# Kernel tuning notes

Measured on AMD Instinct MI355X. Metric: run time of the kernel, lower is better.

The kernel has to match this reference:

```python
import jax, jax.numpy as jnp
import numpy as np
from math import sqrt

IMG_SIZE = 512
FMAP = IMG_SIZE // 32            # 16
RATIOS = (1.0 / 3.0, 0.5, 1.0, 2.0, 3.0)
SCALE = 0.35
N_CLASSES = 21                   # class 0 = background
MIN_SCORE = 0.01
MAX_OVERLAP = 0.45
BATCH = 16


def make_anchors():
    # mirrors DetectionBaseline.create_anchors (cx, cy, w, h in [0,1])
    anchors = []
    for i in range(FMAP):
        for j in range(FMAP):
            cx = (j + 0.5) / FMAP
            cy = (i + 0.5) / FMAP
            for r in RATIOS:
                anchors.append([cx, cy, SCALE * sqrt(r), SCALE / sqrt(r)])
    return jnp.clip(jnp.asarray(anchors, dtype=jnp.float32), 0.0, 1.0)


def setup_inputs() -> dict:
    key = jax.random.key(0)
    k1, k2 = jax.random.split(key)
    A = FMAP * FMAP * len(RATIOS)  # 1280 anchors
    return {
        "predicted_locs": jax.random.normal(k1, (BATCH, A, 4), dtype=jnp.float32),
        "predicted_scores": jax.random.normal(k2, (BATCH, A, N_CLASSES), dtype=jnp.float32),
        "anchors": make_anchors(),
        "top_k": 200,
    }


def _pairwise_iou(boxes):
    # boxes: [B, A, 4] xyxy -> iou [B, A, A]
    area = (boxes[..., 2] - boxes[..., 0]) * (boxes[..., 3] - boxes[..., 1])
    lt = jnp.maximum(boxes[:, :, None, :2], boxes[:, None, :, :2])
    rb = jnp.minimum(boxes[:, :, None, 2:], boxes[:, None, :, 2:])
    wh = jnp.clip(rb - lt, 0.0, None)
    inter = wh[..., 0] * wh[..., 1]
    union = area[:, :, None] + area[:, None, :] - inter
    return inter / union


def reference(predicted_locs, predicted_scores, anchors, top_k):
    B, A, C = predicted_scores.shape
    Cf = C - 1  # foreground classes
    scores = jax.nn.softmax(predicted_scores, axis=2)  # [B, A, C]

    # standard SSD decode (gcxgcywh -> cxcywh -> xyxy)
    cxcy = predicted_locs[..., :2] * anchors[:, 2:] / 10.0 + anchors[:, :2]
    wh = jnp.exp(predicted_locs[..., 2:] / 5.0) * anchors[:, 2:]
    boxes = jnp.concatenate([cxcy - wh / 2.0, cxcy + wh / 2.0], axis=-1)  # [B, A, 4]

    iou = _pairwise_iou(boxes)  # [B, A, A], shared across classes

    cls_scores = jnp.transpose(scores[:, :, 1:], (0, 2, 1))  # [B, Cf, A]
    valid = cls_scores > MIN_SCORE
    order = jnp.argsort(-cls_scores, axis=-1)  # per-class descending score order

    bi = jnp.arange(B)[:, None]   # [B, 1]
    ci = jnp.arange(Cf)[None, :]  # [1, Cf]

    def step(suppress, idx_r):
        # idx_r: [B, Cf] anchor index processed at this rank
        row = iou[bi, idx_r, :] > MAX_OVERLAP            # [B, Cf, A]
        active = (~suppress[bi, ci, idx_r]) & valid[bi, ci, idx_r]  # [B, Cf]
        new = jnp.where(active[..., None], suppress | row, suppress)
        # original sets suppress[box] = 0 after suppressing its overlaps
        new = new.at[bi, ci, idx_r].set(jnp.where(active, False, new[bi, ci, idx_r]))
        return new, None

    suppress0 = jnp.zeros((B, Cf, A), dtype=bool)
    suppress, _ = jax.lax.scan(step, suppress0, jnp.transpose(order, (2, 0, 1)))
    keep = (~suppress) & valid  # [B, Cf, A]

    # gather top_k detections per image across (class, anchor)
    masked = jnp.where(keep, cls_scores, -1.0).reshape(B, Cf * A)
    topv, topi = jax.lax.top_k(masked, top_k)  # [B, top_k]
    cls_idx = topi // A + 1
    anc_idx = topi % A
    det_valid = topv > 0.0
    out_scores = jnp.where(det_valid, topv, 0.0)
    out_labels = jnp.where(det_valid, cls_idx, 0)
    out_boxes = jnp.where(det_valid[..., None], boxes[bi, anc_idx, :], 0.0)
    return out_boxes, out_labels, out_scores
```

## Files before the change

### kernel.cpp

```cpp
#include <hip/hip_runtime.h>
#include <stdint.h>


#define A_N     1280
#define CF      20
#define NC      21
#define B_N     16
#define TOPK    200
#define THREADS 256
#define CTHREADS 512
#define SORT_N  2048
#define CH      128

#define KEYS_BYTES   (B_N * CF * TOPK * 8)
#define BOX_OFF      KEYS_BYTES
#define MS_OFF       (BOX_OFF + B_N * A_N * 16)
#define RANKS_OFF    (MS_OFF + B_N * A_N * 8)
#define WS_B_BYTES   RANKS_OFF
#define WS_A_BYTES   (RANKS_OFF + (size_t)B_N * CF * A_N * 2)

static __device__ __forceinline__ uint64_t pack_key(float sc, uint32_t idx) {
    return ((uint64_t)(uint32_t)(~__float_as_uint(sc)) << 32) | (uint64_t)idx;
}

static __device__ __forceinline__ float box_area(const float4 v) {
    return (v.z - v.x) * (v.w - v.y);
}

static __device__ __forceinline__ bool iou_gt(const float4 a, const float aarea,
                                              const float4 b, const float barea) {
    const float lx = fmaxf(a.x, b.x);
    const float ly = fmaxf(a.y, b.y);
    const float rx = fminf(a.z, b.z);
    const float ry = fminf(a.w, b.w);
    const float wx = fmaxf(rx - lx, 0.0f);
    const float wy = fmaxf(ry - ly, 0.0f);
    const float inter = wx * wy;
    const float uni   = aarea + barea - inter;
    return inter / uni > 0.45f;
}

static __device__ __forceinline__ float4 decode_box(const float4 lc, const float4 an) {
    const float cx = lc.x * an.z / 10.0f + an.x;
    const float cy = lc.y * an.w / 10.0f + an.y;
    const float w  = expf(lc.z / 5.0f) * an.z;
    const float h  = expf(lc.w / 5.0f) * an.w;
    float4 v;
    v.x = cx - w / 2.0f; v.y = cy - h / 2.0f;
    v.z = cx + w / 2.0f; v.w = cy + h / 2.0f;
    return v;
}

static __device__ __forceinline__ float4 shfl_box(const float4 v, int lane) {
    float4 r;
    r.x = __shfl(v.x, lane, 64);
    r.y = __shfl(v.y, lane, 64);
    r.z = __shfl(v.z, lane, 64);
    r.w = __shfl(v.w, lane, 64);
    return r;
}

static __device__ __forceinline__ uint64_t readlane_u64(uint64_t v, int lane) {
    const uint32_t lo = (uint32_t)__builtin_amdgcn_readlane((int)(uint32_t)v, lane);
    const uint32_t hi = (uint32_t)__builtin_amdgcn_readlane((int)(uint32_t)(v >> 32), lane);
    return ((uint64_t)hi << 32) | lo;
}

__global__ __launch_bounds__(THREADS)
void prep_kernel(const float* __restrict__ locs,
                 const float* __restrict__ scores,
                 const float* __restrict__ anchors,
                 float4* __restrict__ boxes_ws,
                 float2* __restrict__ ms_ws)
{
    const int g = blockIdx.x * THREADS + threadIdx.x;
    if (g >= B_N * A_N) return;
    const int a = g % A_N;
    boxes_ws[g] = decode_box(((const float4*)locs)[g], ((const float4*)anchors)[a]);
    const float* sp = scores + (size_t)g * NC;
    float m = sp[0];
    #pragma unroll
    for (int k = 1; k < NC; ++k) m = fmaxf(m, sp[k]);
    float sum = 0.0f;
    #pragma unroll
    for (int k = 0; k < NC; ++k) sum += expf(sp[k] - m);
    ms_ws[g] = make_float2(m, sum);
}

__global__ __launch_bounds__(THREADS)
void sort_kernel(const float* __restrict__ scores,
                 const float2* __restrict__ ms_ws,
                 unsigned short* __restrict__ ranks_ws)
{
    __shared__ uint64_t skeys[SORT_N];

    const int blk = blockIdx.x;
    const int b   = blk / CF;
    const int c   = blk % CF + 1;
    const int t   = threadIdx.x;
    const int l   = t & 63;
    const int w   = t >> 6;

    #pragma unroll
    for (int i = 0; i < A_N / THREADS; ++i) {
        const int a = t + i * THREADS;
        const float2 ms = ms_ws[b * A_N + a];
        const float  sl = scores[((size_t)b * A_N + a) * NC + c];
        const float  sc = expf(sl - ms.x) / ms.y;
        skeys[a] = (sc > 0.01f) ? pack_key(sc, (uint32_t)a) : ~0ull;
    }
    for (int i = A_N + t; i < SORT_N; i += THREADS) skeys[i] = ~0ull;
    __syncthreads();

    uint64_t k[8];
    #pragma unroll
    for (int r = 0; r < 8; ++r) k[r] = skeys[(w << 9) + (r << 6) + l];

    for (int kk = 2; kk <= SORT_N; kk <<= 1) {
        for (int j = kk >> 1; j; j >>= 1) {
            if (j >= 512) {
                __syncthreads();
                #pragma unroll
                for (int r = 0; r < 8; ++r) skeys[(w << 9) + (r << 6) + l] = k[r];
                __syncthreads();
                #pragma unroll
                for (int r = 0; r < 8; ++r) {
                    const int e = (w << 9) + (r << 6) + l;
                    const uint64_t o = skeys[e ^ j];
                    const bool keep_min = (((e & j) == 0) == ((e & kk) == 0));
                    const uint64_t mn = k[r] < o ? k[r] : o;
                    const uint64_t mx = k[r] < o ? o : k[r];
                    k[r] = keep_min ? mn : mx;
                }
            } else if (j >= 64) {
                const int rb = j >> 6;
                #pragma unroll
                for (int r = 0; r < 8; ++r) {
                    if ((r & rb) == 0) {
                        const int p = r | rb;
                        const int e = (w << 9) + (r << 6) + l;
                        const bool up = ((e & kk) == 0);
                        const uint64_t x = k[r], y = k[p];
                        const uint64_t mn = x < y ? x : y;
                        const uint64_t mx = x < y ? y : x;
                        k[r] = up ? mn : mx;
                        k[p] = up ? mx : mn;
                    }
                }
            } else {
                #pragma unroll
                for (int r = 0; r < 8; ++r) {
                    const uint64_t o = (uint64_t)__shfl_xor((unsigned long long)k[r], j, 64);
                    const int e = (w << 9) + (r << 6) + l;
                    const bool keep_min = (((e & j) == 0) == ((e & kk) == 0));
                    const uint64_t mn = k[r] < o ? k[r] : o;
                    const uint64_t mx = k[r] < o ? o : k[r];
                    k[r] = keep_min ? mn : mx;
                }
            }
        }
    }
    unsigned short* const dst = ranks_ws + (size_t)blk * A_N;
    #pragma unroll
    for (int r = 0; r < 8; ++r) {
        const int e = (w << 9) + (r << 6) + l;
        if (e < A_N)
            dst[e] = (k[r] == ~0ull) ? (unsigned short)0xFFFF
                                     : (unsigned short)(k[r] & 0xFFFF);
    }
}

__global__ __launch_bounds__(CTHREADS)
void chunk_nms_kernel(const float* __restrict__ scores,
                      const float2* __restrict__ ms_ws,
                      const float4* __restrict__ boxes_ws,
                      const unsigned short* __restrict__ ranks_ws,
                      uint64_t* __restrict__ ws_keys)
{
    __shared__ unsigned short sranks[A_N];
    __shared__ uint64_t       srow[CH][2];
    __shared__ unsigned char  sdead[CH];
    __shared__ float4         swbox[TOPK];
    __shared__ float          swarea[TOPK];
    __shared__ unsigned short swidx[TOPK];
    __shared__ int            sW;

    const int blk = blockIdx.x;
    const int b   = blk / CF;
    const int c   = blk % CF + 1;
    const int t   = threadIdx.x;
    const int l   = t & 63;
    const int w   = t >> 6;

    const unsigned short* const rsrc = ranks_ws + (size_t)blk * A_N;
    const float4* const bbase = boxes_ws + (size_t)b * A_N;
    for (int i = t; i < A_N; i += CTHREADS) sranks[i] = rsrc[i];
    if (t == 0) sW = 0;
    __syncthreads();

    int W = 0;
    for (int cb = 0; cb < A_N; cb += CH) {
        if (sranks[cb] == 0xFFFF) break;

        const unsigned short rk0 = sranks[cb + l];
        const unsigned short rk1 = sranks[cb + 64 + l];
        const float4 box_lo = (rk0 != 0xFFFF) ? bbase[rk0] : make_float4(-8.f, -8.f, -8.f, -8.f);
        const float4 box_hi = (rk1 != 0xFFFF) ? bbase[rk1] : make_float4(-8.f, -8.f, -8.f, -8.f);
        const float  al = box_area(box_lo);
        const float  ah = box_area(box_hi);

        {
            const int bx = t >> 2, q = t & 3;
            const unsigned short rkx = sranks[cb + bx];
            const bool valid = (rkx != 0xFFFF);
            const float4 bv = valid ? bbase[rkx] : make_float4(-8.f, -8.f, -8.f, -8.f);
            const float  av = box_area(bv);
            int dead = valid ? 0 : 1;
            #pragma unroll 4
            for (int i = q; i < W; i += 4) {
                dead |= iou_gt(swbox[i], swarea[i], bv, av) ? 1 : 0;
            }
            dead |= __shfl_xor(dead, 1, 64);
            dead |= __shfl_xor(dead, 2, 64);
            if (q == 0) sdead[bx] = (unsigned char)dead;
        }
        __syncthreads();

        {
            const int rbase = w * 16;
            uint32_t rm = (uint32_t)__ballot(l < 16 && !sdead[rbase + l]) & 0xFFFFu;
            while (rm) {
                const int j = __ffs(rm) - 1; rm &= rm - 1;
                const int row = rbase + j;
                const float4 rowsrc = (row < 64) ? box_lo : box_hi;
                const float4 rbx = shfl_box(rowsrc, row & 63);
                const float  ra  = box_area(rbx);
                const uint64_t m0 = __ballot(iou_gt(rbx, ra, box_lo, al));
                const uint64_t m1 = __ballot(iou_gt(rbx, ra, box_hi, ah));
                if (l == 0) { srow[row][0] = m0; srow[row][1] = m1; }
            }
        }
        __syncthreads();

        if (w == 0) {
            const uint64_t r0lo = srow[l][0];
            const uint64_t r0hi = srow[l][1];
            const uint64_t r1lo = srow[64 + l][0];
            const uint64_t r1hi = srow[64 + l][1];
            uint64_t alive0 = __ballot(sdead[l] == 0);
            uint64_t alive1 = __ballot(sdead[64 + l] == 0);
            int Wl = W;
            while ((alive0 | alive1) && Wl < TOPK) {
                const int f = alive0 ? __builtin_ctzll(alive0)
                                     : 64 + __builtin_ctzll(alive1);
                if (f < 64) {
                    if (l == f)      { swidx[Wl] = rk0; swbox[Wl] = box_lo; swarea[Wl] = al; }
                } else {
                    if (l == f - 64) { swidx[Wl] = rk1; swbox[Wl] = box_hi; swarea[Wl] = ah; }
                }
                uint64_t klo, khi;
                if (f < 64) { klo = readlane_u64(r0lo, f);      khi = readlane_u64(r0hi, f); }
                else        { klo = readlane_u64(r1lo, f - 64); khi = readlane_u64(r1hi, f - 64); }
                alive0 &= ~klo;
                alive1 &= ~khi;
                ++Wl;
            }
            if (l == 0) sW = Wl;
        }
        __syncthreads();
        W = sW;
        if (W >= TOPK) break;
    }

    const uint32_t  base = (uint32_t)(c - 1) * A_N;
    uint64_t* const out  = ws_keys + ((size_t)b * CF + (c - 1)) * TOPK;
    for (int k2 = t; k2 < TOPK; k2 += CTHREADS) {
        if (k2 < W) {
            const int a = swidx[k2];
            const float2 ms = ms_ws[(size_t)b * A_N + a];
            const float  sc = expf(scores[((size_t)b * A_N + a) * NC + c] - ms.x) / ms.y;
            out[k2] = ((uint64_t)(uint32_t)(~__float_as_uint(sc)) << 32)
                    | (uint64_t)(base + (uint32_t)a);
        } else {
            out[k2] = ~0ull;
        }
    }
}

template <bool PREP>
__global__ __launch_bounds__(THREADS)
void nms_mono(const float* __restrict__ locs,
              const float* __restrict__ scores,
              const float* __restrict__ anchors,
              const float4* __restrict__ boxes_ws,
              const float2* __restrict__ ms_ws,
              uint64_t* __restrict__ ws_keys)
{
    __shared__ uint64_t      skeys[SORT_N];
    __shared__ float4        sbox[A_N];
    __shared__ float4        schunk[CH];
    __shared__ uint64_t      srow[CH][2];
    __shared__ float4        swbox[TOPK];
    __shared__ uint64_t      swkey[TOPK];
    __shared__ unsigned char sdead[CH];
    __shared__ int           sW;

    const int blk = blockIdx.x;
    const int b   = blk / CF;
    const int c   = blk % CF + 1;
    const int t   = threadIdx.x;
    const int l   = t & 63;
    const int w   = t >> 6;

    #pragma unroll
    for (int i = 0; i < A_N / THREADS; ++i) {
        const int a = t + i * THREADS;
        float4 v; float m, sum;
        if (PREP) {
            v = boxes_ws[b * A_N + a];
            const float2 ms = ms_ws[b * A_N + a];
            m = ms.x; sum = ms.y;
        } else {
            v = decode_box(((const float4*)locs)[(size_t)b * A_N + a],
                           ((const float4*)anchors)[a]);
            const float* sp = scores + ((size_t)b * A_N + a) * NC;
            m = sp[0];
            #pragma unroll
            for (int k = 1; k < NC; ++k) m = fmaxf(m, sp[k]);
            sum = 0.0f;
            #pragma unroll
            for (int k = 0; k < NC; ++k) sum += expf(sp[k] - m);
        }
        sbox[a] = v;
        const float sl = scores[((size_t)b * A_N + a) * NC + c];
        const float sc = expf(sl - m) / sum;
        skeys[a] = (sc > 0.01f) ? pack_key(sc, (uint32_t)a) : ~0ull;
    }
    for (int i = A_N + t; i < SORT_N; i += THREADS) skeys[i] = ~0ull;
    if (t == 0) sW = 0;
    __syncthreads();

    uint64_t k[8];
    #pragma unroll
    for (int r = 0; r < 8; ++r) k[r] = skeys[(w << 9) + (r << 6) + l];
    for (int kk = 2; kk <= SORT_N; kk <<= 1) {
        for (int j = kk >> 1; j; j >>= 1) {
            if (j >= 512) {
                __syncthreads();
                #pragma unroll
                for (int r = 0; r < 8; ++r) skeys[(w << 9) + (r << 6) + l] = k[r];
                __syncthreads();
                #pragma unroll
                for (int r = 0; r < 8; ++r) {
                    const int e = (w << 9) + (r << 6) + l;
                    const uint64_t o = skeys[e ^ j];
                    const bool keep_min = (((e & j) == 0) == ((e & kk) == 0));
                    const uint64_t mn = k[r] < o ? k[r] : o;
                    const uint64_t mx = k[r] < o ? o : k[r];
                    k[r] = keep_min ? mn : mx;
                }
            } else if (j >= 64) {
                const int rb = j >> 6;
                #pragma unroll
                for (int r = 0; r < 8; ++r) {
                    if ((r & rb) == 0) {
                        const int p = r | rb;
                        const int e = (w << 9) + (r << 6) + l;
                        const bool up = ((e & kk) == 0);
                        const uint64_t x = k[r], y = k[p];
                        const uint64_t mn = x < y ? x : y;
                        const uint64_t mx = x < y ? y : x;
                        k[r] = up ? mn : mx;
                        k[p] = up ? mx : mn;
                    }
                }
            } else {
                #pragma unroll
                for (int r = 0; r < 8; ++r) {
                    const uint64_t o = (uint64_t)__shfl_xor((unsigned long long)k[r], j, 64);
                    const int e = (w << 9) + (r << 6) + l;
                    const bool keep_min = (((e & j) == 0) == ((e & kk) == 0));
                    const uint64_t mn = k[r] < o ? k[r] : o;
                    const uint64_t mx = k[r] < o ? o : k[r];
                    k[r] = keep_min ? mn : mx;
                }
            }
        }
    }
    __syncthreads();
    #pragma unroll
    for (int r = 0; r < 8; ++r) skeys[(w << 9) + (r << 6) + l] = k[r];
    __syncthreads();

    int W = 0;
    for (int cb = 0; cb < SORT_N; cb += CH) {
        if (skeys[cb] == ~0ull) break;
        if (t < CH) {
            const uint64_t kc = skeys[cb + t];
            const bool v = (kc != ~0ull);
            schunk[t] = v ? sbox[(uint32_t)kc] : make_float4(-8.f, -8.f, -8.f, -8.f);
            sdead[t]  = v ? 0 : 1;
        }
        __syncthreads();
        const float4 cb0 = schunk[l];
        const float4 cb1 = schunk[64 + l];
        const float  ca0 = box_area(cb0);
        const float  ca1 = box_area(cb1);
        for (int r = w * 32; r < w * 32 + 32; ++r) {
            const float4 rbx = schunk[r];
            const float  ra  = box_area(rbx);
            const uint64_t m0 = __ballot(iou_gt(rbx, ra, cb0, ca0));
            const uint64_t m1 = __ballot(iou_gt(rbx, ra, cb1, ca1));
            if (l == 0) { srow[r][0] = m0; srow[r][1] = m1; }
        }
        {
            const int jj = t >> 1, h = t & 1;
            const float4 bj = schunk[jj];
            const float  aj = box_area(bj);
            int sup = 0;
            for (int w2 = h; w2 < W; w2 += 2) {
                const float4 bw = swbox[w2];
                if (iou_gt(bw, box_area(bw), bj, aj)) { sup = 1; break; }
            }
            sup |= __shfl_xor(sup, 1, 64);
            if (h == 0 && sup) sdead[jj] = 1;
        }
        __syncthreads();
        if (t < 64) {
            bool al0 = !sdead[t];
            bool al1 = !sdead[64 + t];
            int Wl = W;
            while (true) {
                const unsigned long long bal0 = __ballot(al0);
                const unsigned long long bal1 = __ballot(al1);
                if (!(bal0 | bal1)) break;
                const int f = bal0 ? (__ffsll(bal0) - 1) : (64 + __ffsll(bal1) - 1);
                if (t == 0) { swkey[Wl] = skeys[cb + f]; swbox[Wl] = schunk[f]; }
                const uint64_t r0 = srow[f][0];
                const uint64_t r1 = srow[f][1];
                al0 = al0 && !((r0 >> t) & 1);
                al1 = al1 && !((r1 >> t) & 1);
                if (++Wl >= TOPK) break;
            }
            if (t == 0) sW = Wl;
        }
        __syncthreads();
        W = sW;
        if (W >= TOPK) break;
    }

    const uint32_t  base = (uint32_t)(c - 1) * A_N;
    uint64_t* const out  = ws_keys + ((size_t)b * CF + (c - 1)) * TOPK;
    for (int kx = t; kx < TOPK; kx += THREADS) {
        if (kx < W) {
            const uint64_t kk2 = swkey[kx];
            out[kx] = (kk2 & 0xFFFFFFFF00000000ull) | (uint64_t)(base + (uint32_t)kk2);
        } else {
            out[kx] = ~0ull;
        }
    }
}

__global__ __launch_bounds__(THREADS)
void merge_kernel(const float* __restrict__ locs,
                  const float* __restrict__ anchors,
                  const uint64_t* __restrict__ ws_keys,
                  float* __restrict__ out)
{
    __shared__ uint64_t Abuf[20][256];
    __shared__ uint64_t Bbuf[10][256];

    const int b = blockIdx.x;
    const int t = threadIdx.x;
    const uint64_t* const in = ws_keys + (size_t)b * CF * TOPK;

    for (int e = t; e < CF * 256; e += THREADS) {
        const int c = e >> 8, i = e & 255;
        Abuf[c][i] = (i < TOPK) ? in[c * TOPK + i] : ~0ull;
    }

    uint64_t (*src)[256] = Abuf;
    uint64_t (*dst)[256] = Bbuf;
    int n = CF;
    while (n > 1) {
        const int  nm    = n >> 1;
        const bool carry = (n & 1) != 0;
        __syncthreads();
        for (int e = t; e < nm * 256; e += THREADS) {
            const int mm = e >> 8, i = e & 255;
            const uint64_t x = src[2 * mm][i];
            const uint64_t y = src[2 * mm + 1][255 - i];
            dst[mm][i] = x < y ? x : y;
        }
        if (carry)
            for (int i = t; i < 256; i += THREADS) dst[nm][i] = src[n - 1][i];
        for (int j = 128; j; j >>= 1) {
            __syncthreads();
            for (int pp = t; pp < nm * 128; pp += THREADS) {
                const int mm = pp >> 7, qq = pp & 127;
                const int i  = ((qq & ~(j - 1)) << 1) | (qq & (j - 1));
                const uint64_t x = dst[mm][i], y = dst[mm][i + j];
                if (y < x) { dst[mm][i] = y; dst[mm][i + j] = x; }
            }
        }
        uint64_t (*tmp)[256] = src; src = dst; dst = tmp;
        n = nm + (carry ? 1 : 0);
    }
    __syncthreads();

    if (t < TOPK) {
        const uint64_t k = src[0][t];
        float* const boxes_out  = out;
        float* const labels_out = out + (size_t)B_N * TOPK * 4;
        float* const scores_out = out + (size_t)B_N * TOPK * 5;
        const size_t s = (size_t)b * TOPK + t;
        if (k == ~0ull) {
            boxes_out[s * 4 + 0] = 0.0f;
            boxes_out[s * 4 + 1] = 0.0f;
            boxes_out[s * 4 + 2] = 0.0f;
            boxes_out[s * 4 + 3] = 0.0f;
            labels_out[s] = 0.0f;
            scores_out[s] = 0.0f;
        } else {
            const uint32_t flat = (uint32_t)k;
            const int cls = flat / A_N;
            const int a   = flat - cls * A_N;
            const float sc = __uint_as_float(~(uint32_t)(k >> 32));
            const float4 v = decode_box(((const float4*)locs)[(size_t)b * A_N + a],
                                        ((const float4*)anchors)[a]);
            boxes_out[s * 4 + 0] = v.x;
            boxes_out[s * 4 + 1] = v.y;
            boxes_out[s * 4 + 2] = v.z;
            boxes_out[s * 4 + 3] = v.w;
            labels_out[s] = (float)(cls + 1);
            scores_out[s] = sc;
        }
    }
}

extern "C" void kernel_launch(void* const* d_in, const int* in_sizes, int n_in,
                              void* d_out, int out_size, void* d_ws, size_t ws_size,
                              hipStream_t stream) {
    const float* locs    = (const float*)d_in[0];
    const float* scores  = (const float*)d_in[1];
    const float* anchors = (const float*)d_in[2];
    uint64_t*       ws_keys  = (uint64_t*)d_ws;
    float4*         boxes_ws = (float4*)((char*)d_ws + BOX_OFF);
    float2*         ms_ws    = (float2*)((char*)d_ws + MS_OFF);
    unsigned short* ranks_ws = (unsigned short*)((char*)d_ws + RANKS_OFF);
    float*          outp     = (float*)d_out;

    if (ws_size >= WS_A_BYTES) {
        hipLaunchKernelGGL(prep_kernel, dim3((B_N * A_N + THREADS - 1) / THREADS),
                           dim3(THREADS), 0, stream, locs, scores, anchors, boxes_ws, ms_ws);
        hipLaunchKernelGGL(sort_kernel, dim3(B_N * CF), dim3(THREADS), 0, stream,
                           scores, ms_ws, ranks_ws);
        hipLaunchKernelGGL(chunk_nms_kernel, dim3(B_N * CF), dim3(CTHREADS), 0, stream,
                           scores, ms_ws, boxes_ws, ranks_ws, ws_keys);
    } else if (ws_size >= WS_B_BYTES) {
        hipLaunchKernelGGL(prep_kernel, dim3((B_N * A_N + THREADS - 1) / THREADS),
                           dim3(THREADS), 0, stream, locs, scores, anchors, boxes_ws, ms_ws);
        hipLaunchKernelGGL((nms_mono<true>), dim3(B_N * CF), dim3(THREADS), 0, stream,
                           locs, scores, anchors, boxes_ws, ms_ws, ws_keys);
    } else {
        hipLaunchKernelGGL((nms_mono<false>), dim3(B_N * CF), dim3(THREADS), 0, stream,
                           locs, scores, anchors, boxes_ws, ms_ws, ws_keys);
    }
    hipLaunchKernelGGL(merge_kernel, dim3(B_N), dim3(THREADS), 0, stream,
                       locs, anchors, ws_keys, outp);
}
```

Baseline: 180.4 us.

## Precompute per-image IoU bitmask shared across classes for chunked NMS

Adds a kernel that computes, once per image, a bit matrix of pairwise IoU > threshold between all anchors' decoded boxes. A new chunked NMS kernel then looks up suppression bits from this matrix instead of recomputing box IoUs for each of the 20 classes. This trades redundant arithmetic for scattered global memory reads and an extra launch, and it is only used when the workspace is large enough to hold the matrix.

```diff
diff --git a/kernel.cpp b/kernel.cpp
--- a/kernel.cpp
+++ b/kernel.cpp
@@ -11,6 +11,7 @@
 #define CTHREADS 512
 #define SORT_N  2048
 #define CH      128
+#define IOU_WPR (A_N / 64)
 
 #define KEYS_BYTES   (B_N * CF * TOPK * 8)
 #define BOX_OFF      KEYS_BYTES
@@ -18,6 +19,8 @@
 #define RANKS_OFF    (MS_OFF + B_N * A_N * 8)
 #define WS_B_BYTES   RANKS_OFF
 #define WS_A_BYTES   (RANKS_OFF + (size_t)B_N * CF * A_N * 2)
+#define IOU_OFF      WS_A_BYTES
+#define WS_C_BYTES   (IOU_OFF + (size_t)B_N * A_N * IOU_WPR * 8)
 
 static __device__ __forceinline__ uint64_t pack_key(float sc, uint32_t idx) {
     return ((uint64_t)(uint32_t)(~__float_as_uint(sc)) << 32) | (uint64_t)idx;
@@ -85,6 +88,28 @@
     #pragma unroll
     for (int k = 0; k < NC; ++k) sum += expf(sp[k] - m);
     ms_ws[g] = make_float2(m, sum);
+}
+
+__global__ __launch_bounds__(THREADS)
+void iou_kernel(const float4* __restrict__ boxes_ws,
+                uint64_t* __restrict__ iou_ws)
+{
+    const int t  = threadIdx.x, l = t & 63, w = t >> 6;
+    const int gw = blockIdx.x * (THREADS / 64) + w;
+    const int rs = gw % 10;
+    const int cw = (gw / 10) % IOU_WPR;
+    const int b  = gw / (10 * IOU_WPR);
+    const float4* const bb = boxes_ws + (size_t)b * A_N;
+    const float4 cbx = bb[cw * 64 + l];
+    const float  ca  = box_area(cbx);
+    uint64_t* const obase = iou_ws + (size_t)b * A_N * IOU_WPR + cw;
+    const int r0 = rs * 128;
+    for (int r = r0; r < r0 + 128; ++r) {
+        const float4 rbx = bb[r];
+        const float  ra  = box_area(rbx);
+        const uint64_t m = __ballot(iou_gt(rbx, ra, cbx, ca));
+        if (l == 0) obase[(size_t)r * IOU_WPR] = m;
+    }
 }
 
 __global__ __launch_bounds__(THREADS)
@@ -171,6 +196,120 @@
 }
 
 __global__ __launch_bounds__(CTHREADS)
+void chunk_nms_iou_kernel(const float* __restrict__ scores,
+                          const float2* __restrict__ ms_ws,
+                          const unsigned short* __restrict__ ranks_ws,
+                          const uint64_t* __restrict__ iou_ws,
+                          uint64_t* __restrict__ ws_keys)
+{
+    __shared__ unsigned short sranks[A_N];
+    __shared__ uint64_t       srow[CH][2];
+    __shared__ unsigned char  sdead[CH];
+    __shared__ unsigned short swidx[TOPK];
+    __shared__ int            sW;
+
+    const int blk = blockIdx.x;
+    const int b   = blk / CF;
+    const int c   = blk % CF + 1;
+    const int t   = threadIdx.x;
+    const int l   = t & 63;
+    const int w   = t >> 6;
+
+    const unsigned short* const rsrc = ranks_ws + (size_t)blk * A_N;
+    const uint64_t* const ioub = iou_ws + (size_t)b * A_N * IOU_WPR;
+    for (int i = t; i < A_N; i += CTHREADS) sranks[i] = rsrc[i];
+    if (t == 0) sW = 0;
+    __syncthreads();
+
+    int W = 0;
+    for (int cb = 0; cb < A_N; cb += CH) {
+        if (sranks[cb] == 0xFFFF) break;
+
+        const unsigned short rk0 = sranks[cb + l];
+        const unsigned short rk1 = sranks[cb + 64 + l];
+
+        {
+            const int bx = t >> 2, q = t & 3;
+            const unsigned short rkx = sranks[cb + bx];
+            const bool valid = (rkx != 0xFFFF);
+            const int cwi = valid ? (rkx >> 6) : 0;
+            const int cbi = rkx & 63;
+            int dead = valid ? 0 : 1;
+            #pragma unroll 4
+            for (int i = q; i < W; i += 4) {
+                const int wa = swidx[i];
+                dead |= (int)((ioub[(size_t)wa * IOU_WPR + cwi] >> cbi) & 1);
+            }
+            dead |= __shfl_xor(dead, 1, 64);
+            dead |= __shfl_xor(dead, 2, 64);
+            if (q == 0) sdead[bx] = (unsigned char)dead;
+        }
+        __syncthreads();
+
+        {
+            const bool v0 = (rk0 != 0xFFFF), v1 = (rk1 != 0xFFFF);
+            const int cw0 = v0 ? (rk0 >> 6) : 0, cb0 = rk0 & 63;
+            const int cw1 = v1 ? (rk1 >> 6) : 0, cb1 = rk1 & 63;
+            const int rbase = w * 16;
+            uint32_t rm = (uint32_t)__ballot(l < 16 && !sdead[rbase + l]) & 0xFFFFu;
+            while (rm) {
+                const int j = __ffs(rm) - 1; rm &= rm - 1;
+                const int row = rbase + j;
+                const unsigned short ra = sranks[cb + row];
+                const uint64_t* const rr = ioub + (size_t)ra * IOU_WPR;
+                const uint64_t m0 = __ballot(((rr[cw0] >> cb0) & 1) != 0);
+                const uint64_t m1 = __ballot(((rr[cw1] >> cb1) & 1) != 0);
+                if (l == 0) { srow[row][0] = m0; srow[row][1] = m1; }
+            }
+        }
+        __syncthreads();
+
+        if (w == 0) {
+            const uint64_t r0lo = srow[l][0];
+            const uint64_t r0hi = srow[l][1];
+            const uint64_t r1lo = srow[64 + l][0];
+            const uint64_t r1hi = srow[64 + l][1];
+            uint64_t alive0 = __ballot(sdead[l] == 0);
+            uint64_t alive1 = __ballot(sdead[64 + l] == 0);
+            int Wl = W;
+            while ((alive0 | alive1) && Wl < TOPK) {
+                const int f = alive0 ? __builtin_ctzll(alive0)
+                                     : 64 + __builtin_ctzll(alive1);
+                if (f < 64) {
+                    if (l == f)      swidx[Wl] = rk0;
+                } else {
+                    if (l == f - 64) swidx[Wl] = rk1;
+                }
+                uint64_t klo, khi;
+                if (f < 64) { klo = readlane_u64(r0lo, f);      khi = readlane_u64(r0hi, f); }
+                else        { klo = readlane_u64(r1lo, f - 64); khi = readlane_u64(r1hi, f - 64); }
+                alive0 &= ~klo;
+                alive1 &= ~khi;
+                ++Wl;
+            }
+            if (l == 0) sW = Wl;
+        }
+        __syncthreads();
+        W = sW;
+        if (W >= TOPK) break;
+    }
+
+    const uint32_t  base = (uint32_t)(c - 1) * A_N;
+    uint64_t* const out  = ws_keys + ((size_t)b * CF + (c - 1)) * TOPK;
+    for (int k2 = t; k2 < TOPK; k2 += CTHREADS) {
+        if (k2 < W) {
+            const int a = swidx[k2];
+            const float2 ms = ms_ws[(size_t)b * A_N + a];
+            const float  sc = expf(scores[((size_t)b * A_N + a) * NC + c] - ms.x) / ms.y;
+            out[k2] = ((uint64_t)(uint32_t)(~__float_as_uint(sc)) << 32)
+                    | (uint64_t)(base + (uint32_t)a);
+        } else {
+            out[k2] = ~0ull;
+        }
+    }
+}
+
+__global__ __launch_bounds__(CTHREADS)
 void chunk_nms_kernel(const float* __restrict__ scores,
                       const float2* __restrict__ ms_ws,
                       const float4* __restrict__ boxes_ws,
@@ -201,14 +340,12 @@
     int W = 0;
     for (int cb = 0; cb < A_N; cb += CH) {
         if (sranks[cb] == 0xFFFF) break;
-
         const unsigned short rk0 = sranks[cb + l];
         const unsigned short rk1 = sranks[cb + 64 + l];
         const float4 box_lo = (rk0 != 0xFFFF) ? bbase[rk0] : make_float4(-8.f, -8.f, -8.f, -8.f);
         const float4 box_hi = (rk1 != 0xFFFF) ? bbase[rk1] : make_float4(-8.f, -8.f, -8.f, -8.f);
         const float  al = box_area(box_lo);
         const float  ah = box_area(box_hi);
-
         {
             const int bx = t >> 2, q = t & 3;
             const unsigned short rkx = sranks[cb + bx];
@@ -225,7 +362,6 @@
             if (q == 0) sdead[bx] = (unsigned char)dead;
         }
         __syncthreads();
-
         {
             const int rbase = w * 16;
             uint32_t rm = (uint32_t)__ballot(l < 16 && !sdead[rbase + l]) & 0xFFFFu;
@@ -241,7 +377,6 @@
             }
         }
         __syncthreads();
-
         if (w == 0) {
             const uint64_t r0lo = srow[l][0];
             const uint64_t r0hi = srow[l][1];
@@ -548,9 +683,19 @@
     float4*         boxes_ws = (float4*)((char*)d_ws + BOX_OFF);
     float2*         ms_ws    = (float2*)((char*)d_ws + MS_OFF);
     unsigned short* ranks_ws = (unsigned short*)((char*)d_ws + RANKS_OFF);
+    uint64_t*       iou_ws   = (uint64_t*)((char*)d_ws + IOU_OFF);
     float*          outp     = (float*)d_out;
 
-    if (ws_size >= WS_A_BYTES) {
+    if (ws_size >= WS_C_BYTES) {
+        hipLaunchKernelGGL(prep_kernel, dim3((B_N * A_N + THREADS - 1) / THREADS),
+                           dim3(THREADS), 0, stream, locs, scores, anchors, boxes_ws, ms_ws);
+        hipLaunchKernelGGL(iou_kernel, dim3(B_N * IOU_WPR * 10 / (THREADS / 64)),
+                           dim3(THREADS), 0, stream, boxes_ws, iou_ws);
+        hipLaunchKernelGGL(sort_kernel, dim3(B_N * CF), dim3(THREADS), 0, stream,
+                           scores, ms_ws, ranks_ws);
+        hipLaunchKernelGGL(chunk_nms_iou_kernel, dim3(B_N * CF), dim3(CTHREADS), 0, stream,
+                           scores, ms_ws, ranks_ws, iou_ws, ws_keys);
+    } else if (ws_size >= WS_A_BYTES) {
         hipLaunchKernelGGL(prep_kernel, dim3((B_N * A_N + THREADS - 1) / THREADS),
                            dim3(THREADS), 0, stream, locs, scores, anchors, boxes_ws, ms_ws);
         hipLaunchKernelGGL(sort_kernel, dim3(B_N * CF), dim3(THREADS), 0, stream,
```

New measurement: 241.9 us. 34.1% more time.

## Fuse per-class sort and chunked NMS into one 512-thread kernel

Applied to the files above, without the earlier changes.

Merges the separate bitonic sort kernel and the chunked NMS kernel into a single 512-thread kernel. The sorted keys stay in shared memory instead of a ranks array being written to and reread from global memory, which also removes one launch. The kept keys are stored directly, so the score is no longer recomputed at output. The sort now runs with 4 keys per thread across 8 waves, which needs more block-wide barriers (j>=256) but uses more threads. Shared memory per block grows because skeys and the NMS buffers coexist.

```diff
diff --git a/kernel.cpp b/kernel.cpp
--- a/kernel.cpp
+++ b/kernel.cpp
@@ -15,9 +15,7 @@
 #define KEYS_BYTES   (B_N * CF * TOPK * 8)
 #define BOX_OFF      KEYS_BYTES
 #define MS_OFF       (BOX_OFF + B_N * A_N * 16)
-#define RANKS_OFF    (MS_OFF + B_N * A_N * 8)
-#define WS_B_BYTES   RANKS_OFF
-#define WS_A_BYTES   (RANKS_OFF + (size_t)B_N * CF * A_N * 2)
+#define WS_B_BYTES   (MS_OFF + B_N * A_N * 8)
 
 static __device__ __forceinline__ uint64_t pack_key(float sc, uint32_t idx) {
     return ((uint64_t)(uint32_t)(~__float_as_uint(sc)) << 32) | (uint64_t)idx;
@@ -87,12 +85,19 @@
     ms_ws[g] = make_float2(m, sum);
 }
 
-__global__ __launch_bounds__(THREADS)
-void sort_kernel(const float* __restrict__ scores,
-                 const float2* __restrict__ ms_ws,
-                 unsigned short* __restrict__ ranks_ws)
+__global__ __launch_bounds__(CTHREADS)
+void fused_nms_kernel(const float* __restrict__ scores,
+                      const float2* __restrict__ ms_ws,
+                      const float4* __restrict__ boxes_ws,
+                      uint64_t* __restrict__ ws_keys)
 {
-    __shared__ uint64_t skeys[SORT_N];
+    __shared__ uint64_t      skeys[SORT_N];
+    __shared__ uint64_t      srow[CH][2];
+    __shared__ unsigned char sdead[CH];
+    __shared__ float4        swbox[TOPK];
+    __shared__ float         swarea[TOPK];
+    __shared__ uint64_t      swkey[TOPK];
+    __shared__ int           sW;
 
     const int blk = blockIdx.x;
     const int b   = blk / CF;
@@ -102,30 +107,34 @@
     const int w   = t >> 6;
 
     #pragma unroll
-    for (int i = 0; i < A_N / THREADS; ++i) {
-        const int a = t + i * THREADS;
-        const float2 ms = ms_ws[b * A_N + a];
-        const float  sl = scores[((size_t)b * A_N + a) * NC + c];
-        const float  sc = expf(sl - ms.x) / ms.y;
-        skeys[a] = (sc > 0.01f) ? pack_key(sc, (uint32_t)a) : ~0ull;
-    }
-    for (int i = A_N + t; i < SORT_N; i += THREADS) skeys[i] = ~0ull;
-    __syncthreads();
-
-    uint64_t k[8];
-    #pragma unroll
-    for (int r = 0; r < 8; ++r) k[r] = skeys[(w << 9) + (r << 6) + l];
+    for (int i = 0; i < SORT_N / CTHREADS; ++i) {
+        const int a = t + i * CTHREADS;
+        if (a < A_N) {
+            const float2 ms = ms_ws[b * A_N + a];
+            const float  sl = scores[((size_t)b * A_N + a) * NC + c];
+            const float  sc = expf(sl - ms.x) / ms.y;
+            skeys[a] = (sc > 0.01f) ? pack_key(sc, (uint32_t)a) : ~0ull;
+        } else {
+            skeys[a] = ~0ull;
+        }
+    }
+    if (t == 0) sW = 0;
+    __syncthreads();
+
+    uint64_t k[4];
+    #pragma unroll
+    for (int r = 0; r < 4; ++r) k[r] = skeys[(w << 8) + (r << 6) + l];
 
     for (int kk = 2; kk <= SORT_N; kk <<= 1) {
         for (int j = kk >> 1; j; j >>= 1) {
-            if (j >= 512) {
+            if (j >= 256) {
                 __syncthreads();
                 #pragma unroll
-                for (int r = 0; r < 8; ++r) skeys[(w << 9) + (r << 6) + l] = k[r];
+                for (int r = 0; r < 4; ++r) skeys[(w << 8) + (r << 6) + l] = k[r];
                 __syncthreads();
                 #pragma unroll
-                for (int r = 0; r < 8; ++r) {
-                    const int e = (w << 9) + (r << 6) + l;
+                for (int r = 0; r < 4; ++r) {
+                    const int e = (w << 8) + (r << 6) + l;
                     const uint64_t o = skeys[e ^ j];
                     const bool keep_min = (((e & j) == 0) == ((e & kk) == 0));
                     const uint64_t mn = k[r] < o ? k[r] : o;
@@ -135,10 +144,10 @@
             } else if (j >= 64) {
                 const int rb = j >> 6;
                 #pragma unroll
-                for (int r = 0; r < 8; ++r) {
+                for (int r = 0; r < 4; ++r) {
                     if ((r & rb) == 0) {
                         const int p = r | rb;
-                        const int e = (w << 9) + (r << 6) + l;
+                        const int e = (w << 8) + (r << 6) + l;
                         const bool up = ((e & kk) == 0);
                         const uint64_t x = k[r], y = k[p];
                         const uint64_t mn = x < y ? x : y;
@@ -149,9 +158,9 @@
                 }
             } else {
                 #pragma unroll
-                for (int r = 0; r < 8; ++r) {
+                for (int r = 0; r < 4; ++r) {
                     const uint64_t o = (uint64_t)__shfl_xor((unsigned long long)k[r], j, 64);
-                    const int e = (w << 9) + (r << 6) + l;
+                    const int e = (w << 8) + (r << 6) + l;
                     const bool keep_min = (((e & j) == 0) == ((e & kk) == 0));
                     const uint64_t mn = k[r] < o ? k[r] : o;
                     const uint64_t mx = k[r] < o ? o : k[r];
@@ -160,60 +169,29 @@
             }
         }
     }
-    unsigned short* const dst = ranks_ws + (size_t)blk * A_N;
-    #pragma unroll
-    for (int r = 0; r < 8; ++r) {
-        const int e = (w << 9) + (r << 6) + l;
-        if (e < A_N)
-            dst[e] = (k[r] == ~0ull) ? (unsigned short)0xFFFF
-                                     : (unsigned short)(k[r] & 0xFFFF);
-    }
-}
-
-__global__ __launch_bounds__(CTHREADS)
-void chunk_nms_kernel(const float* __restrict__ scores,
-                      const float2* __restrict__ ms_ws,
-                      const float4* __restrict__ boxes_ws,
-                      const unsigned short* __restrict__ ranks_ws,
-                      uint64_t* __restrict__ ws_keys)
-{
-    __shared__ unsigned short sranks[A_N];
-    __shared__ uint64_t       srow[CH][2];
-    __shared__ unsigned char  sdead[CH];
-    __shared__ float4         swbox[TOPK];
-    __shared__ float          swarea[TOPK];
-    __shared__ unsigned short swidx[TOPK];
-    __shared__ int            sW;
-
-    const int blk = blockIdx.x;
-    const int b   = blk / CF;
-    const int c   = blk % CF + 1;
-    const int t   = threadIdx.x;
-    const int l   = t & 63;
-    const int w   = t >> 6;
-
-    const unsigned short* const rsrc = ranks_ws + (size_t)blk * A_N;
+    __syncthreads();
+    #pragma unroll
+    for (int r = 0; r < 4; ++r) skeys[(w << 8) + (r << 6) + l] = k[r];
+    __syncthreads();
+
     const float4* const bbase = boxes_ws + (size_t)b * A_N;
-    for (int i = t; i < A_N; i += CTHREADS) sranks[i] = rsrc[i];
-    if (t == 0) sW = 0;
-    __syncthreads();
-
     int W = 0;
     for (int cb = 0; cb < A_N; cb += CH) {
-        if (sranks[cb] == 0xFFFF) break;
-
-        const unsigned short rk0 = sranks[cb + l];
-        const unsigned short rk1 = sranks[cb + 64 + l];
-        const float4 box_lo = (rk0 != 0xFFFF) ? bbase[rk0] : make_float4(-8.f, -8.f, -8.f, -8.f);
-        const float4 box_hi = (rk1 != 0xFFFF) ? bbase[rk1] : make_float4(-8.f, -8.f, -8.f, -8.f);
+        if (skeys[cb] == ~0ull) break;
+
+        const uint64_t key0 = skeys[cb + l];
+        const uint64_t key1 = skeys[cb + 64 + l];
+        const bool v0 = (key0 != ~0ull), v1 = (key1 != ~0ull);
+        const float4 box_lo = v0 ? bbase[(uint32_t)key0] : make_float4(-8.f, -8.f, -8.f, -8.f);
+        const float4 box_hi = v1 ? bbase[(uint32_t)key1] : make_float4(-8.f, -8.f, -8.f, -8.f);
         const float  al = box_area(box_lo);
         const float  ah = box_area(box_hi);
 
         {
             const int bx = t >> 2, q = t & 3;
-            const unsigned short rkx = sranks[cb + bx];
-            const bool valid = (rkx != 0xFFFF);
-            const float4 bv = valid ? bbase[rkx] : make_float4(-8.f, -8.f, -8.f, -8.f);
+            const uint64_t keyx = skeys[cb + bx];
+            const bool valid = (keyx != ~0ull);
+            const float4 bv = valid ? bbase[(uint32_t)keyx] : make_float4(-8.f, -8.f, -8.f, -8.f);
             const float  av = box_area(bv);
             int dead = valid ? 0 : 1;
             #pragma unroll 4
@@ -254,9 +232,9 @@
                 const int f = alive0 ? __builtin_ctzll(alive0)
                                      : 64 + __builtin_ctzll(alive1);
                 if (f < 64) {
-                    if (l == f)      { swidx[Wl] = rk0; swbox[Wl] = box_lo; swarea[Wl] = al; }
+                    if (l == f)      { swkey[Wl] = key0; swbox[Wl] = box_lo; swarea[Wl] = al; }
                 } else {
-                    if (l == f - 64) { swidx[Wl] = rk1; swbox[Wl] = box_hi; swarea[Wl] = ah; }
+                    if (l == f - 64) { swkey[Wl] = key1; swbox[Wl] = box_hi; swarea[Wl] = ah; }
                 }
                 uint64_t klo, khi;
                 if (f < 64) { klo = readlane_u64(r0lo, f);      khi = readlane_u64(r0hi, f); }
@@ -276,24 +254,18 @@
     uint64_t* const out  = ws_keys + ((size_t)b * CF + (c - 1)) * TOPK;
     for (int k2 = t; k2 < TOPK; k2 += CTHREADS) {
         if (k2 < W) {
-            const int a = swidx[k2];
-            const float2 ms = ms_ws[(size_t)b * A_N + a];
-            const float  sc = expf(scores[((size_t)b * A_N + a) * NC + c] - ms.x) / ms.y;
-            out[k2] = ((uint64_t)(uint32_t)(~__float_as_uint(sc)) << 32)
-                    | (uint64_t)(base + (uint32_t)a);
+            const uint64_t kk2 = swkey[k2];
+            out[k2] = (kk2 & 0xFFFFFFFF00000000ull) | (uint64_t)(base + (uint32_t)kk2);
         } else {
             out[k2] = ~0ull;
         }
     }
 }
 
-template <bool PREP>
 __global__ __launch_bounds__(THREADS)
 void nms_mono(const float* __restrict__ locs,
               const float* __restrict__ scores,
               const float* __restrict__ anchors,
-              const float4* __restrict__ boxes_ws,
-              const float2* __restrict__ ms_ws,
               uint64_t* __restrict__ ws_keys)
 {
     __shared__ uint64_t      skeys[SORT_N];
@@ -315,25 +287,17 @@
     #pragma unroll
     for (int i = 0; i < A_N / THREADS; ++i) {
         const int a = t + i * THREADS;
-        float4 v; float m, sum;
-        if (PREP) {
-            v = boxes_ws[b * A_N + a];
-            const float2 ms = ms_ws[b * A_N + a];
-            m = ms.x; sum = ms.y;
-        } else {
-            v = decode_box(((const float4*)locs)[(size_t)b * A_N + a],
-                           ((const float4*)anchors)[a]);
-            const float* sp = scores + ((size_t)b * A_N + a) * NC;
-            m = sp[0];
-            #pragma unroll
-            for (int k = 1; k < NC; ++k) m = fmaxf(m, sp[k]);
-            sum = 0.0f;
-            #pragma unroll
-            for (int k = 0; k < NC; ++k) sum += expf(sp[k] - m);
-        }
+        const float4 v = decode_box(((const float4*)locs)[(size_t)b * A_N + a],
+                                    ((const float4*)anchors)[a]);
+        const float* sp = scores + ((size_t)b * A_N + a) * NC;
+        float m = sp[0];
+        #pragma unroll
+        for (int kq = 1; kq < NC; ++kq) m = fmaxf(m, sp[kq]);
+        float sum = 0.0f;
+        #pragma unroll
+        for (int kq = 0; kq < NC; ++kq) sum += expf(sp[kq] - m);
         sbox[a] = v;
-        const float sl = scores[((size_t)b * A_N + a) * NC + c];
-        const float sc = expf(sl - m) / sum;
+        const float sc = expf(sp[c] - m) / sum;
         skeys[a] = (sc > 0.01f) ? pack_key(sc, (uint32_t)a) : ~0ull;
     }
     for (int i = A_N + t; i < SORT_N; i += THREADS) skeys[i] = ~0ull;
@@ -544,27 +508,19 @@
     const float* locs    = (const float*)d_in[0];
     const float* scores  = (const float*)d_in[1];
     const float* anchors = (const float*)d_in[2];
-    uint64_t*       ws_keys  = (uint64_t*)d_ws;
-    float4*         boxes_ws = (float4*)((char*)d_ws + BOX_OFF);
-    float2*         ms_ws    = (float2*)((char*)d_ws + MS_OFF);
-    unsigned short* ranks_ws = (unsigned short*)((char*)d_ws + RANKS_OFF);
-    float*          outp     = (float*)d_out;
-
-    if (ws_size >= WS_A_BYTES) {
+    uint64_t* ws_keys  = (uint64_t*)d_ws;
+    float4*   boxes_ws = (float4*)((char*)d_ws + BOX_OFF);
+    float2*   ms_ws    = (float2*)((char*)d_ws + MS_OFF);
+    float*    outp     = (float*)d_out;
+
+    if (ws_size >= (size_t)WS_B_BYTES) {
         hipLaunchKernelGGL(prep_kernel, dim3((B_N * A_N + THREADS - 1) / THREADS),
                            dim3(THREADS), 0, stream, locs, scores, anchors, boxes_ws, ms_ws);
-        hipLaunchKernelGGL(sort_kernel, dim3(B_N * CF), dim3(THREADS), 0, stream,
-                           scores, ms_ws, ranks_ws);
-        hipLaunchKernelGGL(chunk_nms_kernel, dim3(B_N * CF), dim3(CTHREADS), 0, stream,
-                           scores, ms_ws, boxes_ws, ranks_ws, ws_keys);
-    } else if (ws_size >= WS_B_BYTES) {
-        hipLaunchKernelGGL(prep_kernel, dim3((B_N * A_N + THREADS - 1) / THREADS),
-                           dim3(THREADS), 0, stream, locs, scores, anchors, boxes_ws, ms_ws);
-        hipLaunchKernelGGL((nms_mono<true>), dim3(B_N * CF), dim3(THREADS), 0, stream,
-                           locs, scores, anchors, boxes_ws, ms_ws, ws_keys);
+        hipLaunchKernelGGL(fused_nms_kernel, dim3(B_N * CF), dim3(CTHREADS), 0, stream,
+                           scores, ms_ws, boxes_ws, ws_keys);
     } else {
-        hipLaunchKernelGGL((nms_mono<false>), dim3(B_N * CF), dim3(THREADS), 0, stream,
-                           locs, scores, anchors, boxes_ws, ms_ws, ws_keys);
+        hipLaunchKernelGGL(nms_mono, dim3(B_N * CF), dim3(THREADS), 0, stream,
+                           locs, scores, anchors, ws_keys);
     }
     hipLaunchKernelGGL(merge_kernel, dim3(B_N), dim3(THREADS), 0, stream,
                        locs, anchors, ws_keys, outp);
```

After: 171.1 us, median of 2. -5.1%, faster.
